# Kernel tuning notes

Measured on AMD Instinct MI355X. Metric: run time of the kernel, lower is better.

The kernel has to match this reference:

```python
import jax, jax.numpy as jnp
import numpy as np
from jax import lax

B, C_IN, C, H, W = 4, 256, 128, 64, 64
UP = (128, 128)
EPS = 1e-8  # torch CosineSimilarity eps


def _conv(x, w, b, p):
    y = lax.conv_general_dilated(x, w, (1, 1), [(p, p), (p, p)],
                                 dimension_numbers=('NCHW', 'OIHW', 'NCHW'))
    return y + b[None, :, None, None]


def _stdconv(x, w, b, s, o, p=0):
    # StdConv.forward = bn(act(conv(x))); eval-mode BatchNorm folded to per-channel affine (s, o)
    y = jax.nn.relu(_conv(x, w, b, p))
    return y * s[None, :, None, None] + o[None, :, None, None]


def _forward(t1, t2, t1_w, t1_b, t2_w, t2_b,
             df_res_w, df_res_b, df_res_s, df_res_o,
             df_b0_w, df_b0_b, df_b0_s, df_b0_o,
             df_b1_w, df_b1_b, df_b1_s, df_b1_o,
             df_fu_w, df_fu_b, df_fu_s, df_fu_o,
             br1_w, br1_b, br2_w, br2_b,
             fu_w, fu_b, fu_s, fu_o):
    Bs, _, Hs, Ws = t1.shape
    res1 = _conv(t1, t1_w, t1_b, 0)                      # [B,C,H,W]
    res2 = _conv(t2, t2_w, t2_b, 0)
    # torch .contiguous().view(B,-1,c) on NCHW: plain row-major reshape (NOT a transpose)
    f1 = res1.reshape(Bs, Hs * Ws, C)
    f2 = res2.reshape(Bs, Hs * Ws, C)
    num = jnp.sum(f1 * f2, axis=-1)
    den = jnp.maximum(jnp.linalg.norm(f1, axis=-1) * jnp.linalg.norm(f2, axis=-1), EPS)
    sim = (num / den)[..., None]                          # [B,HW,1]
    dif_w = 1.0 - sim

    def to_img(f):  # permute(0,2,1).view(B,C,H,W)
        return jnp.transpose(f, (0, 2, 1)).reshape(Bs, C, Hs, Ws)

    sim1 = to_img(f1 * sim) + res1
    sim2 = to_img(f2 * sim) + res2
    dif1 = to_img(f1 * dif_w) + res1
    dif2 = to_img(f2 * dif_w) + res2
    # AvgPool2d(kernel=2, stride=2)
    simp = jnp.abs(sim1 - sim2).reshape(Bs, C, Hs // 2, 2, Ws // 2, 2).mean(axis=(3, 5))
    # InceptionConv(2C -> C, branch=2)
    x = jnp.concatenate([dif1, dif2], axis=1)
    r = _stdconv(x, df_res_w, df_res_b, df_res_s, df_res_o, 0)
    b0 = _stdconv(r, df_b0_w, df_b0_b, df_b0_s, df_b0_o, 1)   # 3x3
    b1 = _stdconv(r, df_b1_w, df_b1_b, df_b1_s, df_b1_o, 2)   # 5x5
    dif = _stdconv(jnp.concatenate([b0, b1], axis=1), df_fu_w, df_fu_b, df_fu_s, df_fu_o, 0) + r
    N = (Hs // 2) * (Ws // 2)
    attn = simp.reshape(Bs, N, C)                         # [B,N,C]

    def branch_attn(inc):
        br = inc.reshape(Bs, C, Hs * Ws)                  # [B,C,HW]
        a = jax.nn.softmax(jnp.einsum('bnc,bcm->bnm', attn, br), axis=-1)  # [B,N,HW]
        return jnp.einsum('bnc,bnm->bcm', attn, a).reshape(Bs, C, Hs, Ws) + inc

    inc1 = _conv(dif, br1_w, br1_b, 1)
    inc2 = _conv(dif, br2_w, br2_b, 2)
    a1 = branch_attn(inc1)
    a2 = branch_attn(inc2)
    fused = _stdconv(jnp.concatenate([a1, a2], axis=1), fu_w, fu_b, fu_s, fu_o, 0) + dif
    # F.interpolate(..., mode='bilinear', align_corners=False) == jax bilinear resize
    return jax.image.resize(fused, (Bs, C, UP[0], UP[1]), method='bilinear')


def setup_inputs():
    key = jax.random.key(0)
    ks = iter(jax.random.split(key, 40))
    rn = lambda shape, sc=0.05: jax.random.normal(next(ks), shape, jnp.float32) * sc
    return {
        't1': jax.random.normal(next(ks), (B, C_IN, H, W), jnp.float32),
        't2': jax.random.normal(next(ks), (B, C_IN, H, W), jnp.float32),
        't1_w': rn((C, C_IN, 1, 1)), 't1_b': rn((C,)),
        't2_w': rn((C, C_IN, 1, 1)), 't2_b': rn((C,)),
        'df_res_w': rn((C, 2 * C, 1, 1)), 'df_res_b': rn((C,)), 'df_res_s': 1.0 + rn((C,)), 'df_res_o': rn((C,)),
        'df_b0_w': rn((C // 2, C, 3, 3)), 'df_b0_b': rn((C // 2,)), 'df_b0_s': 1.0 + rn((C // 2,)), 'df_b0_o': rn((C // 2,)),
        'df_b1_w': rn((C // 2, C, 5, 5)), 'df_b1_b': rn((C // 2,)), 'df_b1_s': 1.0 + rn((C // 2,)), 'df_b1_o': rn((C // 2,)),
        'df_fu_w': rn((C, C, 1, 1)), 'df_fu_b': rn((C,)), 'df_fu_s': 1.0 + rn((C,)), 'df_fu_o': rn((C,)),
        'br1_w': rn((C, C, 3, 3)), 'br1_b': rn((C,)),
        'br2_w': rn((C, C, 5, 5)), 'br2_b': rn((C,)),
        'fu_w': rn((C, 2 * C, 1, 1)), 'fu_b': rn((C,)), 'fu_s': 1.0 + rn((C,)), 'fu_o': rn((C,)),
    }


def reference(t1, t2, t1_w, t1_b, t2_w, t2_b,
              df_res_w, df_res_b, df_res_s, df_res_o,
              df_b0_w, df_b0_b, df_b0_s, df_b0_o,
              df_b1_w, df_b1_b, df_b1_s, df_b1_o,
              df_fu_w, df_fu_b, df_fu_s, df_fu_o,
              br1_w, br1_b, br2_w, br2_b,
              fu_w, fu_b, fu_s, fu_o):
    return _forward(t1, t2, t1_w, t1_b, t2_w, t2_b,
                    df_res_w, df_res_b, df_res_s, df_res_o,
                    df_b0_w, df_b0_b, df_b0_s, df_b0_o,
                    df_b1_w, df_b1_b, df_b1_s, df_b1_o,
                    df_fu_w, df_fu_b, df_fu_s, df_fu_o,
                    br1_w, br1_b, br2_w, br2_b,
                    fu_w, fu_b, fu_s, fu_o)
```

## Files before the change

### kernel.cpp

```cpp
#include <hip/hip_runtime.h>
#include <math.h>

#define HW 4096

typedef __attribute__((ext_vector_type(8))) short short8;
typedef __attribute__((ext_vector_type(4))) float floatx4;
typedef __attribute__((ext_vector_type(2))) float floatx2;

__device__ inline unsigned short f2bf(float f) {
    unsigned int u = __float_as_uint(f);
    unsigned int r = (u + 0x7fffu + ((u >> 16) & 1u)) >> 16;
    return (unsigned short)r;
}
__device__ inline float bf2f(unsigned short u) {
    return __uint_as_float(((unsigned int)u) << 16);
}


__global__ void zero_kernel(uint4* __restrict__ p, int n)
{
    int i = blockIdx.x * 256 + threadIdx.x;
    if (i < n) p[i] = make_uint4(0u, 0u, 0u, 0u);
}

__global__ void prepack_w(const float* __restrict__ w, unsigned short* __restrict__ wp,
                          int CO, int CI, int KK)
{
    int i = blockIdx.x * 256 + threadIdx.x;
    if (i >= CO * CI * KK) return;
    int ci = i % CI;
    int t = i / CI;
    int co = t % CO;
    int kk = t / CO;
    int ti = (kk * (CO >> 4) + (co >> 4)) * (CI >> 5) + (ci >> 5);
    wp[(size_t)ti * 512 + ((ci >> 3) & 3) * 128 + (co & 15) * 8 + (ci & 7)]
        = f2bf(w[(co * CI + ci) * KK + kk]);
}

__global__ void __launch_bounds__(256)
conv1x1_v2(const float* __restrict__ in, const float* __restrict__ w,
           const float* __restrict__ bias, float* __restrict__ out,
           int CI, int CO, int do_affine,
           const float* __restrict__ s, const float* __restrict__ o,
           const float* __restrict__ addbuf, unsigned short* __restrict__ xt)
{
    __shared__ float wl[2048];
    int tid = threadIdx.x;
    int c0 = blockIdx.y * 8;
    int b = blockIdx.z;
    for (int i = tid; i < CI * 8; i += 256) {
        int k = i & 7, ci = i >> 3;
        wl[i] = w[(c0 + k) * CI + ci];
    }
    __syncthreads();
    int m = blockIdx.x * 512 + tid * 2;
    floatx2 acc[8];
#pragma unroll
    for (int k = 0; k < 8; ++k) {
        float bv = bias[c0 + k];
        acc[k] = (floatx2){bv, bv};
    }
    const float* inb = in + (size_t)b * CI * HW + m;
#pragma unroll 4
    for (int ci = 0; ci < CI; ++ci) {
        floatx2 v = *(const floatx2*)(inb + (size_t)ci * HW);
#pragma unroll
        for (int k = 0; k < 8; ++k) acc[k] += wl[ci * 8 + k] * v;
    }
#pragma unroll
    for (int k = 0; k < 8; ++k) {
        floatx2 v = acc[k];
        if (do_affine) {
            float sc = s[c0 + k], of = o[c0 + k];
            v[0] = fmaxf(v[0], 0.f) * sc + of;
            v[1] = fmaxf(v[1], 0.f) * sc + of;
        }
        size_t oidx = ((size_t)(b * CO + c0 + k)) * HW + m;
        if (addbuf) v += *(const floatx2*)(addbuf + oidx);
        *(floatx2*)(out + oidx) = v;
        acc[k] = v;
    }
    if (xt) {
#pragma unroll
        for (int r = 0; r < 2; ++r) {
            int mm = m + r;
            union { unsigned short u16[8]; uint4 q; } pk;
#pragma unroll
            for (int k = 0; k < 8; ++k) pk.u16[k] = f2bf(acc[k][r]);
            int h = mm >> 6, wc = mm & 63;
            *(uint4*)(xt + ((size_t)(b * 16 + (c0 >> 3)) * 4624 + (h + 2) * 68 + (wc + 2)) * 8) = pk.q;
        }
    }
}

template<int K, int CO, int NB, int MS>
__global__ void __launch_bounds__(256)
convk_mfma(const unsigned short* __restrict__ xt, const unsigned short* __restrict__ wp,
           const float* __restrict__ bias, float* __restrict__ out,
           int OB, int co_off, int do_affine,
           const float* __restrict__ s, const float* __restrict__ o,
           unsigned short* __restrict__ incT)
{
    constexpr int CI = 128;
    constexpr int PAD = K / 2;
    constexpr int RO = 2 - PAD;
    constexpr int MT = 4 / MS;
    constexpr int CO16 = CO >> 4;
    constexpr int CI32 = CI >> 5;
    int tid = threadIdx.x;
    int wave = tid >> 6, lane = tid & 63;
    int h = blockIdx.x / MS, msb = blockIdx.x % MS;
    int b = blockIdx.y;
    int co0 = wave * 16 * NB;
    int n = lane & 15, q = lane >> 4;
    floatx4 acc[MT][NB];
#pragma unroll
    for (int mt = 0; mt < MT; ++mt)
#pragma unroll
        for (int nt = 0; nt < NB; ++nt) acc[mt][nt] = (floatx4){0.f, 0.f, 0.f, 0.f};

    const unsigned short* xb = xt + (size_t)(b * 16) * 4624 * 8;
    int mbase = msb * MT * 16;
    for (int ci0 = 0; ci0 < CI; ci0 += 32) {
#pragma unroll
        for (int kh = 0; kh < K; ++kh) {
            const unsigned short* xrow = xb + (size_t)(((ci0 >> 3) + q) * 4624 + (h + kh + RO) * 68 + RO) * 8;
            const unsigned short* wkh = wp + ((size_t)(kh * K) * CO16 * CI32 + (ci0 >> 5)) * 512 + lane * 8;
#pragma unroll
            for (int kw = 0; kw < K; ++kw) {
                short8 bfr[NB];
#pragma unroll
                for (int nt = 0; nt < NB; ++nt)
                    bfr[nt] = *(const short8*)(wkh + (size_t)((kw * CO16 + (co0 >> 4) + nt) * CI32) * 512);
#pragma unroll
                for (int mt = 0; mt < MT; ++mt) {
                    short8 afr = *(const short8*)(xrow + (mbase + mt * 16 + n + kw) * 8);
#pragma unroll
                    for (int nt = 0; nt < NB; ++nt)
                        acc[mt][nt] = __builtin_amdgcn_mfma_f32_16x16x32_bf16(afr, bfr[nt], acc[mt][nt], 0, 0, 0);
                }
            }
        }
    }
    int px0 = h * 64 + mbase + q * 4;
#pragma unroll
    for (int nt = 0; nt < NB; ++nt) {
        int co = co0 + nt * 16 + n;
        float bi = bias[co];
        float sc = do_affine ? s[co] : 1.f;
        float of = do_affine ? o[co] : 0.f;
        float* ob = out + ((size_t)(b * OB + co_off + co)) * HW;
        unsigned short* tb = incT ? incT + (size_t)b * 524288 : nullptr;
        int cpart = (co >> 5) * 512 + ((co >> 3) & 3) * 128 + (co & 7);
#pragma unroll
        for (int mt = 0; mt < MT; ++mt)
#pragma unroll
            for (int r = 0; r < 4; ++r) {
                int px = px0 + mt * 16 + r;
                float v = acc[mt][nt][r] + bi;
                if (do_affine) v = fmaxf(v, 0.f) * sc + of;
                ob[px] = v;
                if (incT) tb[(size_t)((px >> 4) * 2048 + cpart + (px & 15) * 8)] = f2bf(v);
            }
    }
}

__global__ void sim_kernel(const float* __restrict__ r1, const float* __restrict__ r2,
                           float* __restrict__ sim)
{
    int gw = blockIdx.x * 4 + (threadIdx.x >> 6);
    int lane = threadIdx.x & 63;
    int b = gw >> 12, n = gw & 4095;
    const float* p1 = r1 + (size_t)b * 524288 + (size_t)n * 128;
    const float* p2 = r2 + (size_t)b * 524288 + (size_t)n * 128;
    float a0 = p1[lane], a1 = p1[lane + 64];
    float b0 = p2[lane], b1 = p2[lane + 64];
    float dot = a0 * b0 + a1 * b1;
    float n1 = a0 * a0 + a1 * a1;
    float n2 = b0 * b0 + b1 * b1;
    for (int m = 32; m; m >>= 1) {
        dot += __shfl_xor(dot, m);
        n1  += __shfl_xor(n1, m);
        n2  += __shfl_xor(n2, m);
    }
    if (lane == 0) sim[b * 4096 + n] = dot / fmaxf(sqrtf(n1) * sqrtf(n2), 1e-8f);
}

__global__ void __launch_bounds__(256)
x_kernel2(const float* __restrict__ r1, const float* __restrict__ r2,
          const float* __restrict__ sim, float* __restrict__ xo)
{
    __shared__ float ls1[32 * 129], ls2[32 * 129];
    int b = blockIdx.y, p0 = blockIdx.x * 32, tid = threadIdx.x;
    const float* F1 = r1 + (size_t)b * 524288;
    const float* F2 = r2 + (size_t)b * 524288;
    for (int i = tid; i < 32 * 128; i += 256) {
        int p = i >> 7, c = i & 127;
        ls1[p * 129 + c] = F1[p0 * 128 + i];
        ls2[p * 129 + c] = F2[p0 * 128 + i];
    }
    __syncthreads();
    for (int j = tid; j < 256 * 32; j += 256) {
        int p = j & 31, cc = j >> 5;
        int c = cc & 127;
        float sv = sim[b * 4096 + p0 + p];
        const float* F = (cc & 128) ? F2 : F1;
        float t1v = ((cc & 128) ? ls2 : ls1)[p * 129 + c];
        xo[(size_t)b * 1048576 + (size_t)cc * 4096 + p0 + p] = t1v * (1.f - sv) + F[(size_t)c * 4096 + p0 + p];
    }
}

__global__ void __launch_bounds__(256)
simp_kernel3(const float* __restrict__ r1, const float* __restrict__ r2,
             const float* __restrict__ sim, unsigned short* __restrict__ attn_pk)
{
    __shared__ float lsd[64 * 33];
    int b = blockIdx.y, h2 = blockIdx.x, cg = blockIdx.z, tid = threadIdx.x;
    const float* F1 = r1 + (size_t)b * 524288;
    const float* F2 = r2 + (size_t)b * 524288;
    const float* sb = sim + b * 4096;
    int w2 = tid & 31, cl = tid >> 5;
    float acc[4] = {};
    for (int dh = 0; dh < 2; ++dh) {
        int prow = h2 * 128 + dh * 64;
        __syncthreads();
        for (int i = tid; i < 64 * 32; i += 256) {
            int p = i >> 5, c = i & 31;
            size_t gi = (size_t)(prow + p) * 128 + cg * 32 + c;
            lsd[p * 33 + c] = F1[gi] - F2[gi];
        }
        __syncthreads();
#pragma unroll
        for (int k = 0; k < 4; ++k) {
            int c = cl + 8 * k;
            int cG = cg * 32 + c;
#pragma unroll
            for (int dw = 0; dw < 2; ++dw) {
                int pl = 2 * w2 + dw;
                int p = prow + pl;
                float d = lsd[pl * 33 + c] * sb[p]
                        + (F1[(size_t)cG * 4096 + p] - F2[(size_t)cG * 4096 + p]);
                acc[k] += fabsf(d);
            }
        }
    }
#pragma unroll
    for (int k = 0; k < 4; ++k) {
        int cG = cg * 32 + cl + 8 * k;
        int f = cG * 1024 + h2 * 32 + w2;
        int n = f >> 7, c = f & 127;
        attn_pk[(size_t)b * 131072 + ((n >> 4) * 4 + (c >> 5)) * 512
                + ((c >> 3) & 3) * 128 + (n & 15) * 8 + (c & 7)] = f2bf(acc[k] * 0.25f);
    }
}

__global__ void __launch_bounds__(256)
attnA_pass1(const unsigned short* __restrict__ attn_pk,
            const unsigned short* __restrict__ incT1, const unsigned short* __restrict__ incT2,
            float* __restrict__ pmax, float* __restrict__ psum)
{
    __shared__ float lm[4][16], ls[4][16];
    int pair = blockIdx.y;
    int b = pair & 3, br = pair >> 2;
    int z = blockIdx.z;
    int tid = threadIdx.x;
    int wave = tid >> 6, lane = tid & 63;
    int n0 = blockIdx.x * 16;
    int q = lane >> 4;
    int col = lane & 15;
    const unsigned short* apk = attn_pk + (size_t)b * 131072 + (size_t)blockIdx.x * 2048 + lane * 8;
    short8 afr[4];
#pragma unroll
    for (int kc = 0; kc < 4; ++kc) afr[kc] = *(const short8*)(apk + kc * 512);
    const unsigned short* ibp = (br ? incT2 : incT1) + (size_t)b * 524288 + lane * 8;
    short8 bbuf[2][4];
    {
        const unsigned short* brow = ibp + (size_t)(z * 64 + wave * 16) * 2048;
#pragma unroll
        for (int kc = 0; kc < 4; ++kc) bbuf[0][kc] = *(const short8*)(brow + kc * 512);
        brow += 2048;
#pragma unroll
        for (int kc = 0; kc < 4; ++kc) bbuf[1][kc] = *(const short8*)(brow + kc * 512);
    }
    float rm[4], rs[4];
#pragma unroll
    for (int r = 0; r < 4; ++r) { rm[r] = -3.0e38f; rs[r] = 0.f; }
#pragma unroll
    for (int mt = 0; mt < 16; ++mt) {
        const int cur = mt & 1;
        floatx4 acc = (floatx4){0.f, 0.f, 0.f, 0.f};
#pragma unroll
        for (int kc = 0; kc < 4; ++kc)
            acc = __builtin_amdgcn_mfma_f32_16x16x32_bf16(afr[kc], bbuf[cur][kc], acc, 0, 0, 0);
        if (mt < 14) {
            const unsigned short* brow = ibp + (size_t)(z * 64 + wave * 16 + mt + 2) * 2048;
#pragma unroll
            for (int kc = 0; kc < 4; ++kc) bbuf[cur][kc] = *(const short8*)(brow + kc * 512);
        }
#pragma unroll
        for (int r = 0; r < 4; ++r) {
            float v = acc[r];
            float nm = fmaxf(rm[r], v);
            rs[r] = rs[r] * __expf(rm[r] - nm) + __expf(v - nm);
            rm[r] = nm;
        }
    }
#pragma unroll
    for (int d = 1; d < 16; d <<= 1) {
#pragma unroll
        for (int r = 0; r < 4; ++r) {
            float om = __shfl_xor(rm[r], d);
            float os = __shfl_xor(rs[r], d);
            float nm = fmaxf(rm[r], om);
            rs[r] = rs[r] * __expf(rm[r] - nm) + os * __expf(om - nm);
            rm[r] = nm;
        }
    }
    if (col == 0) {
#pragma unroll
        for (int r = 0; r < 4; ++r) { lm[wave][q * 4 + r] = rm[r]; ls[wave][q * 4 + r] = rs[r]; }
    }
    __syncthreads();
    if (tid < 16) {
        float bm = lm[0][tid], bs = ls[0][tid];
        for (int w = 1; w < 4; ++w) {
            float om = lm[w][tid], os = ls[w][tid];
            float nm = fmaxf(bm, om);
            bs = bs * __expf(bm - nm) + os * __expf(om - nm);
            bm = nm;
        }
        pmax[((size_t)pair * 4 + z) * 1024 + n0 + tid] = bm;
        psum[((size_t)pair * 4 + z) * 1024 + n0 + tid] = bs;
    }
}

__global__ void attnA_merge2(const float* __restrict__ pmax, const float* __restrict__ psum,
                             float* __restrict__ mx, float* __restrict__ rsb)
{
    int i = blockIdx.x * 256 + threadIdx.x;
    int pair = i >> 10, n = i & 1023;
    float bm = pmax[((size_t)pair * 4) * 1024 + n];
    float bs = psum[((size_t)pair * 4) * 1024 + n];
    for (int z = 1; z < 4; ++z) {
        float om = pmax[((size_t)pair * 4 + z) * 1024 + n];
        float os = psum[((size_t)pair * 4 + z) * 1024 + n];
        float nm = fmaxf(bm, om);
        bs = bs * __expf(bm - nm) + os * __expf(om - nm);
        bm = nm;
    }
    mx[i] = bm;
    rsb[i] = 1.f / bs;
}

__global__ void attnA_scale(const unsigned short* __restrict__ attn_pk,
                            const float* __restrict__ rsb, unsigned short* __restrict__ attnS_pk)
{
    int i = blockIdx.x * 256 + threadIdx.x;
    int pair = i >> 17;
    int o = i & 131071;
    int j = o & 7, lane = (o >> 3) & 63, ct = (o >> 9) & 7, kcn = o >> 12;
    int c = ct * 16 + (lane & 15);
    int n = kcn * 32 + (lane >> 4) * 8 + j;
    int b = pair & 3;
    float rc = rsb[pair * 1024 + n];
    int ii = b * 131072 + ((n >> 4) * 4 + (c >> 5)) * 512
           + ((c >> 3) & 3) * 128 + (n & 15) * 8 + (c & 7);
    attnS_pk[(size_t)i] = f2bf(bf2f(attn_pk[ii]) * rc);
}

__global__ void __launch_bounds__(256)
attn_passB4(const unsigned short* __restrict__ attn_pk,
            const unsigned short* __restrict__ attnS_pk,
            const unsigned short* __restrict__ incT1, const unsigned short* __restrict__ incT2,
            const float* __restrict__ mx,
            const float* __restrict__ inc1, const float* __restrict__ inc2,
            float* __restrict__ abuf)
{
    __shared__ unsigned short lp[4][16 * 36];
    __shared__ float lred[2][2048];
    int pair = blockIdx.y;
    int b = pair & 3, br = pair >> 2;
    int tid = threadIdx.x;
    int wv = tid >> 6, lane = tid & 63;
    int q = lane >> 4, col = lane & 15;
    int msub = wv & 1, nh = wv >> 1;
    int m0 = blockIdx.x * 32 + msub * 16;
    int mtg = m0 >> 4;
    const unsigned short* ibp = (br ? incT2 : incT1) + (size_t)b * 524288 + lane * 8;
    short8 bfrS[4];
#pragma unroll
    for (int kc = 0; kc < 4; ++kc)
        bfrS[kc] = *(const short8*)(ibp + (size_t)(mtg * 4 + kc) * 512);
    const float* mxp = mx + pair * 1024 + nh * 512;
    const unsigned short* aspk = attnS_pk + (size_t)pair * 131072 + lane * 8;
    const unsigned short* apk = attn_pk + (size_t)b * 131072 + lane * 8;
    floatx4 oacc[8];
#pragma unroll
    for (int ct = 0; ct < 8; ++ct) oacc[ct] = (floatx4){0.f, 0.f, 0.f, 0.f};
    unsigned short* lw = lp[wv];

    short8 arP[2][2][4];
    short8 asP[2][8];
    floatx4 mxq[2][2];
    floatx4 sacc[2][2];

#pragma unroll
    for (int t = 0; t < 2; ++t)
#pragma unroll
        for (int kc = 0; kc < 4; ++kc)
            arP[0][t][kc] = *(const short8*)(apk + (size_t)(((nh * 32 + t) * 4 + kc)) * 512);
#pragma unroll
    for (int ct = 0; ct < 8; ++ct)
        asP[0][ct] = *(const short8*)(aspk + (size_t)((nh * 16) * 8 + ct) * 512);
#pragma unroll
    for (int t = 0; t < 2; ++t)
        mxq[0][t] = *(const floatx4*)(mxp + t * 16 + q * 4);
#pragma unroll
    for (int t = 0; t < 2; ++t) {
        floatx4 a = (floatx4){0.f, 0.f, 0.f, 0.f};
#pragma unroll
        for (int kc = 0; kc < 4; ++kc)
            a = __builtin_amdgcn_mfma_f32_16x16x32_bf16(arP[0][t][kc], bfrS[kc], a, 0, 0, 0);
        sacc[0][t] = a;
    }
#pragma unroll
    for (int t = 0; t < 2; ++t)
#pragma unroll
        for (int kc = 0; kc < 4; ++kc)
            arP[1][t][kc] = *(const short8*)(apk + (size_t)(((nh * 32 + 2 + t) * 4 + kc)) * 512);

#pragma unroll
    for (int nc = 0; nc < 16; ++nc) {
        const int cur = nc & 1, nxt = cur ^ 1;
#pragma unroll
        for (int t = 0; t < 2; ++t) {
            floatx4 sv = sacc[cur][t];
            floatx4 mv = mxq[cur][t];
            unsigned int p01 = (unsigned int)f2bf(__expf(sv[0] - mv[0]))
                             | ((unsigned int)f2bf(__expf(sv[1] - mv[1])) << 16);
            unsigned int p23 = (unsigned int)f2bf(__expf(sv[2] - mv[2]))
                             | ((unsigned int)f2bf(__expf(sv[3] - mv[3])) << 16);
            *(uint2*)&lw[col * 36 + t * 16 + q * 4] = make_uint2(p01, p23);
        }
        if (nc < 15) {
#pragma unroll
            for (int ct = 0; ct < 8; ++ct)
                asP[nxt][ct] = *(const short8*)(aspk + (size_t)(((nh * 16 + nc + 1) * 8 + ct)) * 512);
#pragma unroll
            for (int t = 0; t < 2; ++t)
                mxq[nxt][t] = *(const floatx4*)(mxp + (nc + 1) * 32 + t * 16 + q * 4);
        }
        short8 pb = *(const short8*)&lw[col * 36 + q * 8];
        if (nc < 15) {
#pragma unroll
            for (int t = 0; t < 2; ++t) {
                floatx4 a = (floatx4){0.f, 0.f, 0.f, 0.f};
#pragma unroll
                for (int kc = 0; kc < 4; ++kc)
                    a = __builtin_amdgcn_mfma_f32_16x16x32_bf16(arP[nxt][t][kc], bfrS[kc], a, 0, 0, 0);
                sacc[nxt][t] = a;
            }
        }
        if (nc < 14) {
#pragma unroll
            for (int t = 0; t < 2; ++t)
#pragma unroll
                for (int kc = 0; kc < 4; ++kc)
                    arP[cur][t][kc] = *(const short8*)(apk + (size_t)(((nh * 32 + (nc + 2) * 2 + t) * 4 + kc)) * 512);
        }
#pragma unroll
        for (int ct = 0; ct < 8; ++ct)
            oacc[ct] = __builtin_amdgcn_mfma_f32_16x16x32_bf16(asP[cur][ct], pb, oacc[ct], 0, 0, 0);
    }

    if (nh == 1) {
        float* lr = lred[msub];
#pragma unroll
        for (int ct = 0; ct < 8; ++ct)
#pragma unroll
            for (int r = 0; r < 4; ++r)
                lr[(ct * 16 + q * 4 + r) * 16 + col] = oacc[ct][r];
    }
    __syncthreads();
    if (nh == 0) {
        const float* lr = lred[msub];
        const float* resid = (br ? inc2 : inc1) + (size_t)b * 524288;
        float* op = abuf + ((size_t)(b * 256 + br * 128)) * 4096;
        int m = m0 + col;
#pragma unroll
        for (int ct = 0; ct < 8; ++ct)
#pragma unroll
            for (int r = 0; r < 4; ++r) {
                int row = ct * 16 + q * 4 + r;
                op[(size_t)row * 4096 + m] = oacc[ct][r] + lr[row * 16 + col]
                                           + resid[(size_t)row * 4096 + m];
            }
    }
}

__global__ void upsample_kernel(const float* __restrict__ in, float* __restrict__ out)
{
    int i = blockIdx.x * 256 + threadIdx.x;
    int x = i & 127, y = (i >> 7) & 127, bc = i >> 14;
    const float* ib = in + (size_t)bc * HW;
    float sy = 0.5f * y - 0.25f;
    float sx = 0.5f * x - 0.25f;
    int y0 = (int)floorf(sy); float ty = sy - y0;
    int x0 = (int)floorf(sx); float tx = sx - x0;
    int y0c = min(max(y0, 0), 63), y1c = min(max(y0 + 1, 0), 63);
    int x0c = min(max(x0, 0), 63), x1c = min(max(x0 + 1, 0), 63);
    float v00 = ib[y0c * 64 + x0c], v01 = ib[y0c * 64 + x1c];
    float v10 = ib[y1c * 64 + x0c], v11 = ib[y1c * 64 + x1c];
    out[i] = (1.f - ty) * ((1.f - tx) * v00 + tx * v01) + ty * ((1.f - tx) * v10 + tx * v11);
}

extern "C" void kernel_launch(void* const* d_in, const int* in_sizes, int n_in,
                              void* d_out, int out_size, void* d_ws, size_t ws_size,
                              hipStream_t stream)
{
    const float* t1       = (const float*)d_in[0];
    const float* t2       = (const float*)d_in[1];
    const float* t1_w     = (const float*)d_in[2];
    const float* t1_b     = (const float*)d_in[3];
    const float* t2_w     = (const float*)d_in[4];
    const float* t2_b     = (const float*)d_in[5];
    const float* df_res_w = (const float*)d_in[6];
    const float* df_res_b = (const float*)d_in[7];
    const float* df_res_s = (const float*)d_in[8];
    const float* df_res_o = (const float*)d_in[9];
    const float* df_b0_w  = (const float*)d_in[10];
    const float* df_b0_b  = (const float*)d_in[11];
    const float* df_b0_s  = (const float*)d_in[12];
    const float* df_b0_o  = (const float*)d_in[13];
    const float* df_b1_w  = (const float*)d_in[14];
    const float* df_b1_b  = (const float*)d_in[15];
    const float* df_b1_s  = (const float*)d_in[16];
    const float* df_b1_o  = (const float*)d_in[17];
    const float* df_fu_w  = (const float*)d_in[18];
    const float* df_fu_b  = (const float*)d_in[19];
    const float* df_fu_s  = (const float*)d_in[20];
    const float* df_fu_o  = (const float*)d_in[21];
    const float* br1_w    = (const float*)d_in[22];
    const float* br1_b    = (const float*)d_in[23];
    const float* br2_w    = (const float*)d_in[24];
    const float* br2_b    = (const float*)d_in[25];
    const float* fu_w     = (const float*)d_in[26];
    const float* fu_b     = (const float*)d_in[27];
    const float* fu_s     = (const float*)d_in[28];
    const float* fu_o     = (const float*)d_in[29];

    float* ws = (float*)d_ws;
    float* res1 = ws;
    float* res2 = ws + 2097152;
    float* xbuf = ws + 4194304;
    float* scr  = ws + 8388608;
    float* abuf = ws + 12582912;
    float* attnS_f = ws + 16777216;
    float* simv = ws + 17301504;
    float* mxb  = ws + 17317888;

    unsigned short* us     = (unsigned short*)scr;
    unsigned short* wp_b0  = us;
    unsigned short* wp_b1  = us + 73728;
    unsigned short* wp_br1 = us + 278528;
    unsigned short* wp_br2 = us + 425984;
    unsigned short* xt_r   = us + 851968;
    unsigned short* xt_dif = us + 3219456;
    unsigned short* incT1  = us + 5586944;
    unsigned short* incT2  = us + 851968;
    unsigned short* attn_bf= us + 7684096;
    float* scrF = scr;
    float* pmaxb = scrF + 4104192;
    float* psumb = scrF + 4136960;
    float* rsb   = scrF + 4169728;
    unsigned short* attnS  = (unsigned short*)attnS_f;

    dim3 blk(256);

    zero_kernel<<<2312, blk, 0, stream>>>((uint4*)xt_r, 591872);
    prepack_w<<<288,  blk, 0, stream>>>(df_b0_w, wp_b0, 64, 128, 9);
    prepack_w<<<800,  blk, 0, stream>>>(df_b1_w, wp_b1, 64, 128, 25);
    prepack_w<<<576,  blk, 0, stream>>>(br1_w, wp_br1, 128, 128, 9);
    prepack_w<<<1600, blk, 0, stream>>>(br2_w, wp_br2, 128, 128, 25);

    conv1x1_v2<<<dim3(8, 16, 4), blk, 0, stream>>>(t1, t1_w, t1_b, res1, 256, 128, 0, nullptr, nullptr, nullptr, nullptr);
    conv1x1_v2<<<dim3(8, 16, 4), blk, 0, stream>>>(t2, t2_w, t2_b, res2, 256, 128, 0, nullptr, nullptr, nullptr, nullptr);
    sim_kernel<<<4096, blk, 0, stream>>>(res1, res2, simv);
    x_kernel2<<<dim3(128, 4), blk, 0, stream>>>(res1, res2, simv, xbuf);
    simp_kernel3<<<dim3(32, 4, 4), blk, 0, stream>>>(res1, res2, simv, attn_bf);
    conv1x1_v2<<<dim3(8, 16, 4), blk, 0, stream>>>(xbuf, df_res_w, df_res_b, res1, 256, 128, 1, df_res_s, df_res_o, nullptr, xt_r);
    convk_mfma<3, 64, 1, 4><<<dim3(256, 4), blk, 0, stream>>>(xt_r, wp_b0, df_b0_b, res2, 128, 0, 1, df_b0_s, df_b0_o, nullptr);
    convk_mfma<5, 64, 1, 4><<<dim3(256, 4), blk, 0, stream>>>(xt_r, wp_b1, df_b1_b, res2, 128, 64, 1, df_b1_s, df_b1_o, nullptr);
    conv1x1_v2<<<dim3(8, 16, 4), blk, 0, stream>>>(res2, df_fu_w, df_fu_b, xbuf, 128, 128, 1, df_fu_s, df_fu_o, res1, xt_dif);
    convk_mfma<3, 128, 2, 4><<<dim3(256, 4), blk, 0, stream>>>(xt_dif, wp_br1, br1_b, res1, 128, 0, 0, nullptr, nullptr, incT1);
    convk_mfma<5, 128, 2, 4><<<dim3(256, 4), blk, 0, stream>>>(xt_dif, wp_br2, br2_b, res2, 128, 0, 0, nullptr, nullptr, incT2);
    attnA_pass1<<<dim3(64, 8, 4), blk, 0, stream>>>(attn_bf, incT1, incT2, pmaxb, psumb);
    attnA_merge2<<<32, blk, 0, stream>>>(pmaxb, psumb, mxb, rsb);
    attnA_scale<<<4096, blk, 0, stream>>>(attn_bf, rsb, attnS);
    attn_passB4<<<dim3(128, 8), blk, 0, stream>>>(attn_bf, attnS, incT1, incT2, mxb, res1, res2, abuf);
    float* dif = xbuf;
    float* fused = xbuf + 2097152;
    conv1x1_v2<<<dim3(8, 16, 4), blk, 0, stream>>>(abuf, fu_w, fu_b, fused, 256, 128, 1, fu_s, fu_o, dif, nullptr);
    upsample_kernel<<<32768, blk, 0, stream>>>(fused, (float*)d_out);
}
```

Baseline: 522.3 us.

## Merge setup kernels, double rows per attention pass-1 block, fold merge into scale

Combines the zero-fill and four weight-prepack launches into one setup kernel. In the attention first pass, each block now processes 32 query rows with two MFMA accumulators that share the loaded key fragments, which halves the grid and the key reloads. The separate merge kernel is removed: the scale kernel recomputes the 4-way softmax partial merge per element and writes the row max. This trades fewer launches and less key traffic for redundant merge arithmetic in the scale kernel and more registers in pass 1.

```diff
diff --git a/kernel.cpp b/kernel.cpp
--- a/kernel.cpp
+++ b/kernel.cpp
@@ -17,16 +17,9 @@
 }
 
 
-__global__ void zero_kernel(uint4* __restrict__ p, int n)
-{
-    int i = blockIdx.x * 256 + threadIdx.x;
-    if (i < n) p[i] = make_uint4(0u, 0u, 0u, 0u);
-}
-
-__global__ void prepack_w(const float* __restrict__ w, unsigned short* __restrict__ wp,
-                          int CO, int CI, int KK)
-{
-    int i = blockIdx.x * 256 + threadIdx.x;
+__device__ inline void prepack_dev(const float* __restrict__ w, unsigned short* __restrict__ wp,
+                                   int CO, int CI, int KK, int i)
+{
     if (i >= CO * CI * KK) return;
     int ci = i % CI;
     int t = i / CI;
@@ -35,6 +28,27 @@
     int ti = (kk * (CO >> 4) + (co >> 4)) * (CI >> 5) + (ci >> 5);
     wp[(size_t)ti * 512 + ((ci >> 3) & 3) * 128 + (co & 15) * 8 + (ci & 7)]
         = f2bf(w[(co * CI + ci) * KK + kk]);
+}
+
+__global__ void setup_kernel(uint4* __restrict__ zp, int zn,
+                             const float* __restrict__ w0, unsigned short* __restrict__ wp0,
+                             const float* __restrict__ w1, unsigned short* __restrict__ wp1,
+                             const float* __restrict__ w2, unsigned short* __restrict__ wp2,
+                             const float* __restrict__ w3, unsigned short* __restrict__ wp3)
+{
+    int bx = blockIdx.x, tid = threadIdx.x;
+    if (bx < 2312) {
+        int i = bx * 256 + tid;
+        if (i < zn) zp[i] = make_uint4(0u, 0u, 0u, 0u);
+    } else if (bx < 2600) {
+        prepack_dev(w0, wp0, 64, 128, 9,  (bx - 2312) * 256 + tid);
+    } else if (bx < 3400) {
+        prepack_dev(w1, wp1, 64, 128, 25, (bx - 2600) * 256 + tid);
+    } else if (bx < 3976) {
+        prepack_dev(w2, wp2, 128, 128, 9, (bx - 3400) * 256 + tid);
+    } else {
+        prepack_dev(w3, wp3, 128, 128, 25,(bx - 3976) * 256 + tid);
+    }
 }
 
 __global__ void __launch_bounds__(256)
@@ -259,19 +273,22 @@
             const unsigned short* __restrict__ incT1, const unsigned short* __restrict__ incT2,
             float* __restrict__ pmax, float* __restrict__ psum)
 {
-    __shared__ float lm[4][16], ls[4][16];
+    __shared__ float lm[4][32], ls[4][32];
     int pair = blockIdx.y;
     int b = pair & 3, br = pair >> 2;
     int z = blockIdx.z;
     int tid = threadIdx.x;
     int wave = tid >> 6, lane = tid & 63;
-    int n0 = blockIdx.x * 16;
+    int n0 = blockIdx.x * 32;
     int q = lane >> 4;
     int col = lane & 15;
-    const unsigned short* apk = attn_pk + (size_t)b * 131072 + (size_t)blockIdx.x * 2048 + lane * 8;
-    short8 afr[4];
-#pragma unroll
-    for (int kc = 0; kc < 4; ++kc) afr[kc] = *(const short8*)(apk + kc * 512);
+    const unsigned short* apk = attn_pk + (size_t)b * 131072 + (size_t)blockIdx.x * 4096 + lane * 8;
+    short8 afrA[4], afrB[4];
+#pragma unroll
+    for (int kc = 0; kc < 4; ++kc) {
+        afrA[kc] = *(const short8*)(apk + kc * 512);
+        afrB[kc] = *(const short8*)(apk + 2048 + kc * 512);
+    }
     const unsigned short* ibp = (br ? incT2 : incT1) + (size_t)b * 524288 + lane * 8;
     short8 bbuf[2][4];
     {
@@ -282,16 +299,19 @@
 #pragma unroll
         for (int kc = 0; kc < 4; ++kc) bbuf[1][kc] = *(const short8*)(brow + kc * 512);
     }
-    float rm[4], rs[4];
-#pragma unroll
-    for (int r = 0; r < 4; ++r) { rm[r] = -3.0e38f; rs[r] = 0.f; }
+    float rmA[4], rsA[4], rmB[4], rsB[4];
+#pragma unroll
+    for (int r = 0; r < 4; ++r) { rmA[r] = -3.0e38f; rsA[r] = 0.f; rmB[r] = -3.0e38f; rsB[r] = 0.f; }
 #pragma unroll
     for (int mt = 0; mt < 16; ++mt) {
         const int cur = mt & 1;
-        floatx4 acc = (floatx4){0.f, 0.f, 0.f, 0.f};
-#pragma unroll
-        for (int kc = 0; kc < 4; ++kc)
-            acc = __builtin_amdgcn_mfma_f32_16x16x32_bf16(afr[kc], bbuf[cur][kc], acc, 0, 0, 0);
+        floatx4 accA = (floatx4){0.f, 0.f, 0.f, 0.f};
+        floatx4 accB = (floatx4){0.f, 0.f, 0.f, 0.f};
+#pragma unroll
+        for (int kc = 0; kc < 4; ++kc) {
+            accA = __builtin_amdgcn_mfma_f32_16x16x32_bf16(afrA[kc], bbuf[cur][kc], accA, 0, 0, 0);
+            accB = __builtin_amdgcn_mfma_f32_16x16x32_bf16(afrB[kc], bbuf[cur][kc], accB, 0, 0, 0);
+        }
         if (mt < 14) {
             const unsigned short* brow = ibp + (size_t)(z * 64 + wave * 16 + mt + 2) * 2048;
 #pragma unroll
@@ -299,29 +319,41 @@
         }
 #pragma unroll
         for (int r = 0; r < 4; ++r) {
-            float v = acc[r];
-            float nm = fmaxf(rm[r], v);
-            rs[r] = rs[r] * __expf(rm[r] - nm) + __expf(v - nm);
-            rm[r] = nm;
+            float vA = accA[r];
+            float nmA = fmaxf(rmA[r], vA);
+            rsA[r] = rsA[r] * __expf(rmA[r] - nmA) + __expf(vA - nmA);
+            rmA[r] = nmA;
+            float vB = accB[r];
+            float nmB = fmaxf(rmB[r], vB);
+            rsB[r] = rsB[r] * __expf(rmB[r] - nmB) + __expf(vB - nmB);
+            rmB[r] = nmB;
         }
     }
 #pragma unroll
     for (int d = 1; d < 16; d <<= 1) {
 #pragma unroll
         for (int r = 0; r < 4; ++r) {
-            float om = __shfl_xor(rm[r], d);
-            float os = __shfl_xor(rs[r], d);
-            float nm = fmaxf(rm[r], om);
-            rs[r] = rs[r] * __expf(rm[r] - nm) + os * __expf(om - nm);
-            rm[r] = nm;
+            float om = __shfl_xor(rmA[r], d);
+            float os = __shfl_xor(rsA[r], d);
+            float nm = fmaxf(rmA[r], om);
+            rsA[r] = rsA[r] * __expf(rmA[r] - nm) + os * __expf(om - nm);
+            rmA[r] = nm;
+            om = __shfl_xor(rmB[r], d);
+            os = __shfl_xor(rsB[r], d);
+            nm = fmaxf(rmB[r], om);
+            rsB[r] = rsB[r] * __expf(rmB[r] - nm) + os * __expf(om - nm);
+            rmB[r] = nm;
         }
     }
     if (col == 0) {
 #pragma unroll
-        for (int r = 0; r < 4; ++r) { lm[wave][q * 4 + r] = rm[r]; ls[wave][q * 4 + r] = rs[r]; }
+        for (int r = 0; r < 4; ++r) {
+            lm[wave][q * 4 + r] = rmA[r];      ls[wave][q * 4 + r] = rsA[r];
+            lm[wave][16 + q * 4 + r] = rmB[r]; ls[wave][16 + q * 4 + r] = rsB[r];
+        }
     }
     __syncthreads();
-    if (tid < 16) {
+    if (tid < 32) {
         float bm = lm[0][tid], bs = ls[0][tid];
         for (int w = 1; w < 4; ++w) {
             float om = lm[w][tid], os = ls[w][tid];
@@ -334,26 +366,9 @@
     }
 }
 
-__global__ void attnA_merge2(const float* __restrict__ pmax, const float* __restrict__ psum,
-                             float* __restrict__ mx, float* __restrict__ rsb)
-{
-    int i = blockIdx.x * 256 + threadIdx.x;
-    int pair = i >> 10, n = i & 1023;
-    float bm = pmax[((size_t)pair * 4) * 1024 + n];
-    float bs = psum[((size_t)pair * 4) * 1024 + n];
-    for (int z = 1; z < 4; ++z) {
-        float om = pmax[((size_t)pair * 4 + z) * 1024 + n];
-        float os = psum[((size_t)pair * 4 + z) * 1024 + n];
-        float nm = fmaxf(bm, om);
-        bs = bs * __expf(bm - nm) + os * __expf(om - nm);
-        bm = nm;
-    }
-    mx[i] = bm;
-    rsb[i] = 1.f / bs;
-}
-
-__global__ void attnA_scale(const unsigned short* __restrict__ attn_pk,
-                            const float* __restrict__ rsb, unsigned short* __restrict__ attnS_pk)
+__global__ void attnA_scale2(const unsigned short* __restrict__ attn_pk,
+                             const float* __restrict__ pmax, const float* __restrict__ psum,
+                             float* __restrict__ mx, unsigned short* __restrict__ attnS_pk)
 {
     int i = blockIdx.x * 256 + threadIdx.x;
     int pair = i >> 17;
@@ -362,7 +377,18 @@
     int c = ct * 16 + (lane & 15);
     int n = kcn * 32 + (lane >> 4) * 8 + j;
     int b = pair & 3;
-    float rc = rsb[pair * 1024 + n];
+    float bm = pmax[((size_t)pair * 4) * 1024 + n];
+    float bs = psum[((size_t)pair * 4) * 1024 + n];
+#pragma unroll
+    for (int z = 1; z < 4; ++z) {
+        float om = pmax[((size_t)pair * 4 + z) * 1024 + n];
+        float os = psum[((size_t)pair * 4 + z) * 1024 + n];
+        float nm = fmaxf(bm, om);
+        bs = bs * __expf(bm - nm) + os * __expf(om - nm);
+        bm = nm;
+    }
+    if (c == 0) mx[pair * 1024 + n] = bm;
+    float rc = 1.f / bs;
     int ii = b * 131072 + ((n >> 4) * 4 + (c >> 5)) * 512
            + ((c >> 3) & 3) * 128 + (n & 15) * 8 + (c & 7);
     attnS_pk[(size_t)i] = f2bf(bf2f(attn_pk[ii]) * rc);
@@ -572,16 +598,13 @@
     float* scrF = scr;
     float* pmaxb = scrF + 4104192;
     float* psumb = scrF + 4136960;
-    float* rsb   = scrF + 4169728;
     unsigned short* attnS  = (unsigned short*)attnS_f;
 
     dim3 blk(256);
 
-    zero_kernel<<<2312, blk, 0, stream>>>((uint4*)xt_r, 591872);
-    prepack_w<<<288,  blk, 0, stream>>>(df_b0_w, wp_b0, 64, 128, 9);
-    prepack_w<<<800,  blk, 0, stream>>>(df_b1_w, wp_b1, 64, 128, 25);
-    prepack_w<<<576,  blk, 0, stream>>>(br1_w, wp_br1, 128, 128, 9);
-    prepack_w<<<1600, blk, 0, stream>>>(br2_w, wp_br2, 128, 128, 25);
+    setup_kernel<<<5576, blk, 0, stream>>>((uint4*)xt_r, 591872,
+                                           df_b0_w, wp_b0, df_b1_w, wp_b1,
+                                           br1_w, wp_br1, br2_w, wp_br2);
 
     conv1x1_v2<<<dim3(8, 16, 4), blk, 0, stream>>>(t1, t1_w, t1_b, res1, 256, 128, 0, nullptr, nullptr, nullptr, nullptr);
     conv1x1_v2<<<dim3(8, 16, 4), blk, 0, stream>>>(t2, t2_w, t2_b, res2, 256, 128, 0, nullptr, nullptr, nullptr, nullptr);
@@ -594,9 +617,8 @@
     conv1x1_v2<<<dim3(8, 16, 4), blk, 0, stream>>>(res2, df_fu_w, df_fu_b, xbuf, 128, 128, 1, df_fu_s, df_fu_o, res1, xt_dif);
     convk_mfma<3, 128, 2, 4><<<dim3(256, 4), blk, 0, stream>>>(xt_dif, wp_br1, br1_b, res1, 128, 0, 0, nullptr, nullptr, incT1);
     convk_mfma<5, 128, 2, 4><<<dim3(256, 4), blk, 0, stream>>>(xt_dif, wp_br2, br2_b, res2, 128, 0, 0, nullptr, nullptr, incT2);
-    attnA_pass1<<<dim3(64, 8, 4), blk, 0, stream>>>(attn_bf, incT1, incT2, pmaxb, psumb);
-    attnA_merge2<<<32, blk, 0, stream>>>(pmaxb, psumb, mxb, rsb);
-    attnA_scale<<<4096, blk, 0, stream>>>(attn_bf, rsb, attnS);
+    attnA_pass1<<<dim3(32, 8, 4), blk, 0, stream>>>(attn_bf, incT1, incT2, pmaxb, psumb);
+    attnA_scale2<<<4096, blk, 0, stream>>>(attn_bf, pmaxb, psumb, mxb, attnS);
     attn_passB4<<<dim3(128, 8), blk, 0, stream>>>(attn_bf, attnS, incT1, incT2, mxb, res1, res2, abuf);
     float* dif = xbuf;
     float* fused = xbuf + 2097152;
```

Result: slower. 537.7 us (+2.9%).
